# Performance work log

Hardware: AMD Instinct MI355X
Metric: run time of the kernel (lower is better)

Reference implementation:

```python
import jax, jax.numpy as jnp
import numpy as np

B, NP, L, C, NA = 16, 512, 20, 3, 50
RATIO = 0.8
K = int(np.ceil(RATIO * NP))  # 410 nodes kept per graph
N = B * NP
E = 6 * N
NF, EF = 13, 4
EPS = 1e-5


def _graph_norm(x, w, b, ms):
    # PyG GraphNorm called WITHOUT batch in the source -> single global graph
    mean = x.mean(0)
    out = x - ms * mean
    var = (out * out).mean(0)
    return w * out / jnp.sqrt(var + EPS) + b


def _forward(x, pan_w, lin1_w, lin1_b, norm1_w, norm1_b, norm1_ms,
             pool_p, pool_beta, gat_wl, gat_bl, gat_wr, gat_br, gat_att, gat_bias,
             norm2_w, norm2_b, norm2_ms,
             val1_w, val1_b, val2_w, val2_b, val3_w, val3_b,
             adv1_w, adv1_b, adv2_w, adv2_b, adv3_w, adv3_b,
             edge_index, current_node_ids, action_mask):
    src, dst = edge_index[0], edge_index[1]
    # PANConv builds SparseTensor(row=edge_index[1], col=edge_index[0]) -> row = target
    A = jnp.zeros((B, NP, NP), x.dtype).at[dst // NP, dst % NP, src % NP].set(1.0)
    eyeB = jnp.broadcast_to(jnp.eye(NP, dtype=x.dtype), A.shape)

    # panentropy: M = sum_{i=0..L} w_i * A^i  (dense per graph)
    def step(carry, wi):
        tmp, acc = carry
        tmp = tmp @ A
        return (tmp, acc + wi * tmp), None
    (_, M), _ = jax.lax.scan(step, (eyeB, pan_w[0] * eyeB), pan_w[1:])
    deg = M.sum(-1)                                   # row sums
    dis = jnp.where(deg > 0, 1.0 / jnp.sqrt(deg), 0.0)
    Mn = dis[:, :, None] * M * dis[:, None, :]        # D^-1/2 M D^-1/2

    # conv1: propagate (Mn @ x) then Linear
    x3 = x.reshape(B, NP, NF)
    h = jnp.einsum('bij,bjf->bif', Mn, x3) @ lin1_w + lin1_b   # [B,NP,C]
    x1 = jax.nn.relu(_graph_norm(h.reshape(N, C), norm1_w, norm1_b, norm1_ms))  # [N,C]
    h = x1.reshape(B, NP, C)

    # PANPooling: score = tanh(b0 * <x,p> + b1 * colsum(Mn)); keep top K per graph
    score = jnp.tanh(pool_beta[0] * (h * pool_p).sum(-1) + pool_beta[1] * Mn.sum(-2))
    vals, idx = jax.lax.top_k(score, K)                        # [B,K]
    xp = jnp.take_along_axis(h, idx[:, :, None], axis=1) * vals[..., None]
    Mg = jax.vmap(lambda m, i: m[i][:, i])(Mn, idx)            # filtered adjacency [B,K,K]
    mask = (jnp.swapaxes(Mg, 1, 2) != 0) | jnp.eye(K, dtype=bool)  # mask[b,i,j]: edge j->i (+self loops)

    # GATv2Conv, heads=1, eval mode (no dropout), edge_attr not passed in source
    xl = xp @ gat_wl + gat_bl
    xr = xp @ gat_wr + gat_br
    e = jax.nn.leaky_relu(xr[:, :, None, :] + xl[:, None, :, :], 0.2)  # [B,i,j,C]
    logits = jnp.where(mask, jnp.einsum('bijc,c->bij', e, gat_att), -1e9)
    alpha = jax.nn.softmax(logits, axis=-1)
    g = jnp.einsum('bij,bjc->bic', alpha, xl) + gat_bias

    g = jax.nn.relu(_graph_norm(g.reshape(B * K, C), norm2_w, norm2_b, norm2_ms)).reshape(B, K, C)
    gp = g.sum(1)                                              # global_add_pool [B,C]

    # source uses POOLED bincount cumsum offsets to index the pre-pool arrays (faithful)
    gidx = current_node_ids + jnp.arange(B, dtype=current_node_ids.dtype) * K
    feat = jnp.concatenate([x[gidx], x1[gidx], gp], axis=1)    # [B,19]

    a = jax.nn.relu(feat @ adv1_w + adv1_b)
    a = jax.nn.relu(a @ adv2_w + adv2_b)
    a = a @ adv3_w + adv3_b
    v = jax.nn.relu(feat @ val1_w + val1_b)
    v = jax.nn.relu(v @ val2_w + val2_b)
    v = v @ val3_w + val3_b
    q = v + (a - a.mean(1, keepdims=True))
    return jnp.where(action_mask == 0, -1e8, q)


def setup_inputs() -> dict:
    key = jax.random.key(0)
    ks = list(jax.random.split(key, 40))
    nk = lambda: ks.pop()
    # within-graph random edges so the PyG-style batch structure is valid
    g = jax.random.randint(nk(), (E,), 0, B)
    u = jax.random.randint(nk(), (E,), 0, NP)
    v = jax.random.randint(nk(), (E,), 0, NP)
    edge_index = jnp.stack([g * NP + u, g * NP + v]).astype(jnp.int32)

    def lin(k, i, o):
        k1, k2 = jax.random.split(k)
        return (jax.random.normal(k1, (i, o), jnp.float32) / np.sqrt(i),
                jax.random.normal(k2, (o,), jnp.float32) * 0.01)

    lin1_w, lin1_b = lin(nk(), NF, C)
    gat_wl, gat_bl = lin(nk(), C, C)
    gat_wr, gat_br = lin(nk(), C, C)
    val1_w, val1_b = lin(nk(), 19, 10)
    val2_w, val2_b = lin(nk(), 10, 5)
    val3_w, val3_b = lin(nk(), 5, 1)
    adv1_w, adv1_b = lin(nk(), 19, 10)
    adv2_w, adv2_b = lin(nk(), 10, 5)
    adv3_w, adv3_b = lin(nk(), 5, NA)
    return dict(
        x=jax.random.normal(nk(), (N, NF), jnp.float32),
        edge_index=edge_index,
        edge_attr=jax.random.normal(nk(), (E, EF), jnp.float32),
        batch=jnp.arange(N, dtype=jnp.int32) // NP,
        current_node_ids=jax.random.randint(nk(), (B,), 0, NP),
        action_mask=jax.random.randint(nk(), (B, NA), 0, 2),
        pan_w=jax.random.uniform(nk(), (L + 1,), jnp.float32) * 0.5,
        lin1_w=lin1_w, lin1_b=lin1_b,
        norm1_w=jnp.ones(C), norm1_b=jnp.zeros(C), norm1_ms=jnp.ones(C),
        pool_p=jax.random.normal(nk(), (C,), jnp.float32),
        pool_beta=jnp.array([0.5, 0.5], jnp.float32),
        gat_wl=gat_wl, gat_bl=gat_bl, gat_wr=gat_wr, gat_br=gat_br,
        gat_att=jax.random.normal(nk(), (C,), jnp.float32),
        gat_bias=jax.random.normal(nk(), (C,), jnp.float32) * 0.01,
        norm2_w=jnp.ones(C), norm2_b=jnp.zeros(C), norm2_ms=jnp.ones(C),
        val1_w=val1_w, val1_b=val1_b, val2_w=val2_w, val2_b=val2_b,
        val3_w=val3_w, val3_b=val3_b,
        adv1_w=adv1_w, adv1_b=adv1_b, adv2_w=adv2_w, adv2_b=adv2_b,
        adv3_w=adv3_w, adv3_b=adv3_b,
    )


def reference(x, edge_index, edge_attr, batch, current_node_ids, action_mask,
              pan_w, lin1_w, lin1_b, norm1_w, norm1_b, norm1_ms,
              pool_p, pool_beta, gat_wl, gat_bl, gat_wr, gat_br, gat_att, gat_bias,
              norm2_w, norm2_b, norm2_ms,
              val1_w, val1_b, val2_w, val2_b, val3_w, val3_b,
              adv1_w, adv1_b, adv2_w, adv2_b, adv3_w, adv3_b):
    del edge_attr, batch  # received by the torch forward but never consumed
    return _forward(x, pan_w, lin1_w, lin1_b, norm1_w, norm1_b, norm1_ms,
                    pool_p, pool_beta, gat_wl, gat_bl, gat_wr, gat_br, gat_att, gat_bias,
                    norm2_w, norm2_b, norm2_ms,
                    val1_w, val1_b, val2_w, val2_b, val3_w, val3_b,
                    adv1_w, adv1_b, adv2_w, adv2_b, adv3_w, adv3_b,
                    edge_index, current_node_ids, action_mask)
```

## Files before the change

kernel.cpp:

```cpp
#include <hip/hip_runtime.h>
#include <hip/hip_bf16.h>
#include <stdint.h>
#include <math.h>

#define BB   16
#define NPn  512
#define LLp  20
#define NAa  50
#define KKk  410
#define NNt  (BB * NPn)
#define EEe  (6 * NNt)
#define NFf  13
#define KPAD 416
#define KP2  448
#define EPSf 1e-5f
#define QCLMP 1e6f
#define MAXD 28
#define PADR 512

__device__ __forceinline__ float r17_sane(float v) {
    if (!(v == v)) return 0.0f;
    return fminf(fmaxf(v, -1e15f), 1e15f);
}

__global__ __launch_bounds__(256) void r17_scatter(
    const int* __restrict__ ei,
    uint32_t* __restrict__ fwdb, uint32_t* __restrict__ trsb)
{
    const int e = blockIdx.x * 256 + threadIdx.x;
    if (e < EEe) {
        const int src = ei[e], dst = ei[EEe + e];
        atomicOr(&fwdb[(size_t)dst * 16 + ((src & 511) >> 5)], 1u << (src & 31));
        atomicOr(&trsb[(size_t)src * 16 + ((dst & 511) >> 5)], 1u << (dst & 31));
    }
}

__global__ __launch_bounds__(256) void r17_extract(
    const uint32_t* __restrict__ fwdb, const uint32_t* __restrict__ trsb,
    unsigned short* __restrict__ csrF, unsigned short* __restrict__ csrT)
{
    const int t = blockIdx.x * 256 + threadIdx.x;
    const int node = t & 8191;
    const uint32_t* bs = (t < 8192) ? (fwdb + (size_t)node * 16)
                                    : (trsb + (size_t)node * 16);
    unsigned short* cs = (t < 8192) ? csrF : csrT;
    int cnt = 0;
    for (int w = 0; w < 16; ++w) {
        uint32_t bits = bs[w];
        while (bits) {
            const int u = (w << 5) + __ffs(bits) - 1;
            bits &= bits - 1;
            if (cnt < MAXD) cs[(size_t)cnt * 8192 + node] = (unsigned short)u;
            ++cnt;
        }
    }
    for (int j = cnt; j < MAXD; ++j) cs[(size_t)j * 8192 + node] = PADR;
}

__global__ __launch_bounds__(512) void r17_mid(
    const float* __restrict__ x,
    const unsigned short* __restrict__ csrF,
    const unsigned short* __restrict__ csrT,
    const float* __restrict__ panw,
    const float* __restrict__ l1w, const float* __restrict__ l1b,
    float* __restrict__ h_raw, float* __restrict__ colsum,
    uint32_t* __restrict__ Rb)
{
    __shared__ __align__(16) uint32_t sbuf[1047];
    float* pa  = (float*)sbuf;
    float* pb  = (float*)(sbuf + 513);
    float* wsh = (float*)(sbuf + 1026);
    const int b = blockIdx.x, y = blockIdx.y, t = threadIdx.x;
    const int node = b * 512 + t;

    if (y < 4) {
        const int c = y;
        int iF[MAXD];
#pragma unroll
        for (int j = 0; j < MAXD; ++j) iF[j] = (int)csrF[(size_t)j * 8192 + node];
        if (t < 21) wsh[t] = panw[t];

        pa[t] = 1.0f;
        if (t == 0) { pa[512] = 0.0f; pb[512] = 0.0f; }
        __syncthreads();
        float dacc = wsh[0];
        {
            float* rp = pa; float* rn = pb;
            for (int i = 1; i <= LLp; ++i) {
                float tv[MAXD];
#pragma unroll
                for (int j = 0; j < MAXD; ++j) tv[j] = rp[iF[j]];
                float s = 0.0f;
#pragma unroll
                for (int j = 0; j < MAXD; ++j) s += tv[j];
                rn[t] = s;
                dacc += wsh[i] * s;
                __syncthreads();
                float* tp = rp; rp = rn; rn = tp;
            }
        }
        const float d0 = (dacc > 0.0f) ? 1.0f / sqrtf(dacc) : 0.0f;

        int idx[MAXD];
        if (c == 3) {
#pragma unroll
            for (int j = 0; j < MAXD; ++j) idx[j] = (int)csrT[(size_t)j * 8192 + node];
        } else {
#pragma unroll
            for (int j = 0; j < MAXD; ++j) idx[j] = iF[j];
        }
        float seed;
        if (c < 3) {
            float xw = 0.0f;
            const float* xr = x + (size_t)node * NFf;
            for (int f = 0; f < NFf; ++f) xw += xr[f] * l1w[f * 3 + c];
            seed = d0 * xw;
        } else {
            seed = d0;
        }
        pa[t] = seed;
        if (t == 0) { pa[512] = 0.0f; pb[512] = 0.0f; }
        __syncthreads();
        float acc = wsh[0] * seed;
        {
            float* rp = pa; float* rn = pb;
            for (int i = 1; i <= LLp; ++i) {
                float tv[MAXD];
#pragma unroll
                for (int j = 0; j < MAXD; ++j) tv[j] = rp[idx[j]];
                float s = 0.0f;
#pragma unroll
                for (int j = 0; j < MAXD; ++j) s += tv[j];
                rn[t] = s;
                acc += wsh[i] * s;
                __syncthreads();
                float* tp = rp; rp = rn; rn = tp;
            }
        }
        if (c < 3) h_raw[(size_t)node * 3 + c] = r17_sane(d0 * acc + l1b[c]);
        else       colsum[node] = r17_sane(d0 * acc);
    } else {
        const int q = y - 4;
        int iF[MAXD];
#pragma unroll
        for (int j = 0; j < MAXD; ++j) iF[j] = (int)csrF[(size_t)j * 8192 + node];
        uint32_t* R1 = sbuf;
        uint32_t* R2 = sbuf + 513;
        R1[t] = ((t >> 5) == q) ? (1u << (t & 31)) : 0u;
        if (t == 0) { R1[512] = 0u; R2[512] = 0u; }
        __syncthreads();
        uint32_t* Rp = R1; uint32_t* Rn = R2;
        for (int i = 0; i < LLp; ++i) {
            uint32_t tv[MAXD];
#pragma unroll
            for (int j = 0; j < MAXD; ++j) tv[j] = Rp[iF[j]];
            uint32_t r = Rp[t];
#pragma unroll
            for (int j = 0; j < MAXD; ++j) r |= tv[j];
            Rn[t] = r;
            __syncthreads();
            uint32_t* tp = Rp; Rp = Rn; Rn = tp;
        }
        Rb[(size_t)node * 16 + q] = Rp[t];
    }
}

__global__ __launch_bounds__(512) void r18_pool(
    const float* __restrict__ h_raw,
    const float* __restrict__ colsum,
    const uint32_t* __restrict__ Rb,
    const float* n1w, const float* n1b, const float* n1ms,
    const float* poolp, const float* poolb,
    const float* gwl, const float* gbl,
    float* __restrict__ x1,
    float* __restrict__ xpg,
    float* __restrict__ xlg,
    int*   __restrict__ kidxg,
    uint32_t* __restrict__ RTg)
{
    __shared__ __align__(16) uint32_t pg[2208];
    float* sc   = (float*)pg;
    float* mv   = (float*)(pg + 512);
    float* wred = (float*)(pg + 520);
    float* xpS  = (float*)(pg + 544);
    int*   kidx = (int*)(pg + 1792);
    const int b = blockIdx.x, t = threadIdx.x;
    const int lane = t & 63, wv = t >> 6;
    const float inv_n = 1.0f / (float)NNt;

    float hv0[16], hv1[16], hv2[16];
    float p0 = 0.0f, p1 = 0.0f, p2 = 0.0f;
#pragma unroll
    for (int k = 0; k < 16; ++k) {
        const float* hr = h_raw + (size_t)(k * 512 + t) * 3;
        hv0[k] = hr[0]; hv1[k] = hr[1]; hv2[k] = hr[2];
        p0 += hv0[k]; p1 += hv1[k]; p2 += hv2[k];
    }
#pragma unroll
    for (int off = 32; off; off >>= 1) {
        p0 += __shfl_xor(p0, off); p1 += __shfl_xor(p1, off); p2 += __shfl_xor(p2, off);
    }
    if (lane == 0) { wred[wv * 3 + 0] = p0; wred[wv * 3 + 1] = p1; wred[wv * 3 + 2] = p2; }
    __syncthreads();
    if (t < 3) {
        float s = 0.0f;
        for (int w = 0; w < 8; ++w) s += wred[w * 3 + t];
        mv[t] = s * inv_n;
    }
    __syncthreads();
    const float mm0 = n1ms[0] * mv[0], mm1 = n1ms[1] * mv[1], mm2 = n1ms[2] * mv[2];
    float q0 = 0.0f, q1 = 0.0f, q2 = 0.0f;
#pragma unroll
    for (int k = 0; k < 16; ++k) {
        const float d0 = hv0[k] - mm0, d1 = hv1[k] - mm1, d2 = hv2[k] - mm2;
        q0 += d0 * d0; q1 += d1 * d1; q2 += d2 * d2;
    }
#pragma unroll
    for (int off = 32; off; off >>= 1) {
        q0 += __shfl_xor(q0, off); q1 += __shfl_xor(q1, off); q2 += __shfl_xor(q2, off);
    }
    if (lane == 0) { wred[wv * 3 + 0] = q0; wred[wv * 3 + 1] = q1; wred[wv * 3 + 2] = q2; }
    __syncthreads();
    if (t < 3) {
        float s = 0.0f;
        for (int w = 0; w < 8; ++w) s += wred[w * 3 + t];
        mv[3 + t] = s * inv_n;
    }
    __syncthreads();

    const float mmv[3] = { mm0, mm1, mm2 };
    float xv[3];
#pragma unroll
    for (int c = 0; c < 3; ++c) {
        const float iv = 1.0f / sqrtf(fmaxf(mv[3 + c], 0.0f) + EPSf);
        const float o  = h_raw[(size_t)(b * NPn + t) * 3 + c] - mmv[c];
        const float tt = n1w[c] * o * iv + n1b[c];
        xv[c] = fmaxf(tt, 0.0f);
        x1[(size_t)(b * NPn + t) * 3 + c] = xv[c];
    }
    float s = poolb[0] * (xv[0] * poolp[0] + xv[1] * poolp[1] + xv[2] * poolp[2])
            + poolb[1] * colsum[b * NPn + t];
    s = tanhf(s);
    if (!(s == s)) s = 0.0f;
    sc[t] = s;
    __syncthreads();

    int cnt = 0;
    for (int u = 0; u < NPn; u += 4) {
        const float4 s4 = *(const float4*)(sc + u);
        cnt += ((s4.x > s) || (s4.x == s && (u + 0) < t)) ? 1 : 0;
        cnt += ((s4.y > s) || (s4.y == s && (u + 1) < t)) ? 1 : 0;
        cnt += ((s4.z > s) || (s4.z == s && (u + 2) < t)) ? 1 : 0;
        cnt += ((s4.w > s) || (s4.w == s && (u + 3) < t)) ? 1 : 0;
    }
    if (cnt < KKk) {
        const float xp0 = xv[0] * s, xp1 = xv[1] * s, xp2 = xv[2] * s;
        kidx[cnt] = t;
        xpS[cnt * 3 + 0] = xp0;
        xpS[cnt * 3 + 1] = xp1;
        xpS[cnt * 3 + 2] = xp2;
        kidxg[b * KPAD + cnt] = t;
        xpg[(size_t)(b * KPAD + cnt) * 3 + 0] = xp0;
        xpg[(size_t)(b * KPAD + cnt) * 3 + 1] = xp1;
        xpg[(size_t)(b * KPAD + cnt) * 3 + 2] = xp2;
    }
    __syncthreads();

    float Wl[9];
#pragma unroll
    for (int i2 = 0; i2 < 9; ++i2) Wl[i2] = gwl[i2];
    const float Bl0 = gbl[0], Bl1 = gbl[1], Bl2 = gbl[2];
    if (t < KP2) {
        float xl0, xl1, xl2;
        uint32_t* RT = RTg + (size_t)b * 16 * KP2 + t;
        if (t < KKk) {
            const float c0 = xpS[t * 3 + 0];
            const float c1 = xpS[t * 3 + 1];
            const float c2 = xpS[t * 3 + 2];
            xl0 = c0 * Wl[0] + c1 * Wl[3] + c2 * Wl[6] + Bl0;
            xl1 = c0 * Wl[1] + c1 * Wl[4] + c2 * Wl[7] + Bl1;
            xl2 = c0 * Wl[2] + c1 * Wl[5] + c2 * Wl[8] + Bl2;
            const uint4* rr = (const uint4*)(Rb + (size_t)(b * NPn + kidx[t]) * 16);
            const uint4 r0 = rr[0], r1 = rr[1], r2 = rr[2], r3 = rr[3];
            RT[ 0 * KP2] = r0.x; RT[ 1 * KP2] = r0.y; RT[ 2 * KP2] = r0.z; RT[ 3 * KP2] = r0.w;
            RT[ 4 * KP2] = r1.x; RT[ 5 * KP2] = r1.y; RT[ 6 * KP2] = r1.z; RT[ 7 * KP2] = r1.w;
            RT[ 8 * KP2] = r2.x; RT[ 9 * KP2] = r2.y; RT[10 * KP2] = r2.z; RT[11 * KP2] = r2.w;
            RT[12 * KP2] = r3.x; RT[13 * KP2] = r3.y; RT[14 * KP2] = r3.z; RT[15 * KP2] = r3.w;
        } else {
            xl0 = 0.0f; xl1 = 0.0f; xl2 = 0.0f;
#pragma unroll
            for (int w = 0; w < 16; ++w) RT[w * KP2] = 0u;
        }
        xlg[(size_t)(b * KP2 + t) * 3 + 0] = xl0;
        xlg[(size_t)(b * KP2 + t) * 3 + 1] = xl1;
        xlg[(size_t)(b * KP2 + t) * 3 + 2] = xl2;
    }
}

__global__ __launch_bounds__(512) void r18_gat(
    const float* __restrict__ xpg,
    const float* __restrict__ xlg,
    const int* __restrict__ kidxg,
    const uint32_t* __restrict__ RTg,
    const float* __restrict__ gwr, const float* __restrict__ gbr,
    const float* __restrict__ gatt, const float* __restrict__ gbias,
    float* __restrict__ g_raw)
{
    const int b = blockIdx.x, y = blockIdx.y, t = threadIdx.x;
    const int lane = t & 63, wv = t >> 6;
    const int i = y * 8 + wv;
    if (i >= KKk) return;

    float Wr[9];
#pragma unroll
    for (int k = 0; k < 9; ++k) Wr[k] = gwr[k];
    const float Br0 = gbr[0], Br1 = gbr[1], Br2 = gbr[2];
    const float At0 = gatt[0], At1 = gatt[1], At2 = gatt[2];
    const float Gb0 = gbias[0], Gb1 = gbias[1], Gb2 = gbias[2];

    const int bi = kidxg[b * KPAD + i];
    const float c0 = xpg[(size_t)(b * KPAD + i) * 3 + 0];
    const float c1 = xpg[(size_t)(b * KPAD + i) * 3 + 1];
    const float c2 = xpg[(size_t)(b * KPAD + i) * 3 + 2];
    const float xr0 = c0 * Wr[0] + c1 * Wr[3] + c2 * Wr[6] + Br0;
    const float xr1 = c0 * Wr[1] + c1 * Wr[4] + c2 * Wr[7] + Br1;
    const float xr2 = c0 * Wr[2] + c1 * Wr[5] + c2 * Wr[8] + Br2;

    const uint32_t mbit = 1u << (bi & 31);
    const uint32_t* Rw = RTg + (size_t)(b * 16 + (bi >> 5)) * KP2;
    const float* xlb = xlg + (size_t)b * KP2 * 3;

    float mx = -3e38f, lsum = 0.0f, b0 = 0.0f, b1 = 0.0f, b2 = 0.0f;
#pragma unroll
    for (int it = 0; it < 7; ++it) {
        const int j = lane + it * 64;
        const uint32_t rw = Rw[j];
        const float xl0 = xlb[j * 3 + 0];
        const float xl1 = xlb[j * 3 + 1];
        const float xl2 = xlb[j * 3 + 2];
        const bool valid = (rw & mbit) || (j == i);
        float e0 = xr0 + xl0; e0 = e0 > 0.0f ? e0 : 0.2f * e0;
        float e1 = xr1 + xl1; e1 = e1 > 0.0f ? e1 : 0.2f * e1;
        float e2 = xr2 + xl2; e2 = e2 > 0.0f ? e2 : 0.2f * e2;
        const float sv = At0 * e0 + At1 * e1 + At2 * e2;
        if (valid) {
            if (sv > mx) {
                const float r = __expf(mx - sv);
                lsum *= r; b0 *= r; b1 *= r; b2 *= r;
                mx = sv;
            }
            const float pj = __expf(sv - mx);
            lsum += pj;
            b0 += pj * xl0; b1 += pj * xl1; b2 += pj * xl2;
        }
    }
#pragma unroll
    for (int off = 32; off; off >>= 1) {
        const float mo = __shfl_xor(mx, off);
        const float lo = __shfl_xor(lsum, off);
        const float d0 = __shfl_xor(b0, off);
        const float d1 = __shfl_xor(b1, off);
        const float d2 = __shfl_xor(b2, off);
        const float M  = fmaxf(mx, mo);
        const float ea = __expf(mx - M), eb = __expf(mo - M);
        lsum = lsum * ea + lo * eb;
        b0 = b0 * ea + d0 * eb;
        b1 = b1 * ea + d1 * eb;
        b2 = b2 * ea + d2 * eb;
        mx = M;
    }
    if (lane == 0) {
        const float rl = 1.0f / fmaxf(lsum, 1e-30f);
        g_raw[(size_t)(b * KPAD + i) * 3 + 0] = r17_sane(b0 * rl + Gb0);
        g_raw[(size_t)(b * KPAD + i) * 3 + 1] = r17_sane(b1 * rl + Gb1);
        g_raw[(size_t)(b * KPAD + i) * 3 + 2] = r17_sane(b2 * rl + Gb2);
    }
}

__global__ __launch_bounds__(512) void r17_head(
    const float* __restrict__ g_raw,
    const float* __restrict__ x1,
    const float* __restrict__ x,
    const int* __restrict__ cnid,
    const int* __restrict__ amask,
    const float* n2w, const float* n2b, const float* n2ms,
    const float* v1w, const float* v1b,
    const float* v2w, const float* v2b,
    const float* v3w, const float* v3b,
    const float* a1w, const float* a1b,
    const float* a2w, const float* a2b,
    const float* a3w, const float* a3b,
    float* __restrict__ out)
{
    __shared__ float wred[24];
    __shared__ float mv[6];
    __shared__ float gp[3];
    __shared__ float feat[19];
    __shared__ float h1a[10], h1v[10], h2a[5], h2v[5];
    __shared__ float a3[50];
    __shared__ float vout_s, amean_s;
    const int b = blockIdx.x, t = threadIdx.x;
    const int lane = t & 63, wv = t >> 6;
    const float denom = 1.0f / (float)(BB * KKk);

    float gv0[13], gv1[13], gv2[13];
    float p0 = 0.0f, p1 = 0.0f, p2 = 0.0f;
#pragma unroll
    for (int k = 0; k < 13; ++k) {
        const int r = k * 512 + t;
        float q0 = 0.0f, q1 = 0.0f, q2 = 0.0f;
        if (r < BB * KKk) {
            const int bq = r / KKk, iq = r - bq * KKk;
            const float* gr = g_raw + (size_t)(bq * KPAD + iq) * 3;
            q0 = gr[0]; q1 = gr[1]; q2 = gr[2];
        }
        gv0[k] = q0; gv1[k] = q1; gv2[k] = q2;
        p0 += q0; p1 += q1; p2 += q2;
    }
#pragma unroll
    for (int off = 32; off; off >>= 1) {
        p0 += __shfl_xor(p0, off); p1 += __shfl_xor(p1, off); p2 += __shfl_xor(p2, off);
    }
    if (lane == 0) { wred[wv * 3 + 0] = p0; wred[wv * 3 + 1] = p1; wred[wv * 3 + 2] = p2; }
    __syncthreads();
    if (t < 3) {
        float s = 0.0f;
        for (int w = 0; w < 8; ++w) s += wred[w * 3 + t];
        mv[t] = s * denom;
    }
    __syncthreads();
    const float mm0 = n2ms[0] * mv[0], mm1 = n2ms[1] * mv[1], mm2 = n2ms[2] * mv[2];
    float q0a = 0.0f, q1a = 0.0f, q2a = 0.0f;
#pragma unroll
    for (int k = 0; k < 13; ++k) {
        const int r = k * 512 + t;
        if (r < BB * KKk) {
            const float d0 = gv0[k] - mm0, d1 = gv1[k] - mm1, d2 = gv2[k] - mm2;
            q0a += d0 * d0; q1a += d1 * d1; q2a += d2 * d2;
        }
    }
#pragma unroll
    for (int off = 32; off; off >>= 1) {
        q0a += __shfl_xor(q0a, off); q1a += __shfl_xor(q1a, off); q2a += __shfl_xor(q2a, off);
    }
    if (lane == 0) { wred[wv * 3 + 0] = q0a; wred[wv * 3 + 1] = q1a; wred[wv * 3 + 2] = q2a; }
    __syncthreads();
    if (t < 3) {
        float s = 0.0f;
        for (int w = 0; w < 8; ++w) s += wred[w * 3 + t];
        mv[3 + t] = s * denom;
    }
    __syncthreads();

    const float mmv[3] = { mm0, mm1, mm2 };
    float s3[3] = { 0.0f, 0.0f, 0.0f };
    if (t < KKk) {
        const size_t r = (size_t)(b * KPAD + t) * 3;
#pragma unroll
        for (int c = 0; c < 3; ++c) {
            const float iv = 1.0f / sqrtf(fmaxf(mv[3 + c], 0.0f) + EPSf);
            s3[c] = fmaxf((g_raw[r + c] - mmv[c]) * iv * n2w[c] + n2b[c], 0.0f);
        }
    }
    float g0 = s3[0], g1 = s3[1], g2 = s3[2];
#pragma unroll
    for (int off = 32; off; off >>= 1) {
        g0 += __shfl_xor(g0, off); g1 += __shfl_xor(g1, off); g2 += __shfl_xor(g2, off);
    }
    if (lane == 0) { wred[wv * 3 + 0] = g0; wred[wv * 3 + 1] = g1; wred[wv * 3 + 2] = g2; }
    __syncthreads();
    if (t < 3) {
        float s = 0.0f;
        for (int w = 0; w < 8; ++w) s += wred[w * 3 + t];
        gp[t] = s;
    }
    __syncthreads();

    if (t < 19) {
        const int gidx = cnid[b] + b * KKk;
        float fv;
        if (t < 13)      fv = x[(size_t)gidx * NFf + t];
        else if (t < 16) fv = x1[(size_t)gidx * 3 + (t - 13)];
        else             fv = gp[t - 16];
        feat[t] = fv;
    }
    __syncthreads();

    if (t < 10) {
        float s = a1b[t];
        for (int f = 0; f < 19; ++f) s += feat[f] * a1w[f * 10 + t];
        h1a[t] = fmaxf(s, 0.0f);
    } else if (t >= 64 && t < 74) {
        const int j = t - 64;
        float s = v1b[j];
        for (int f = 0; f < 19; ++f) s += feat[f] * v1w[f * 10 + j];
        h1v[j] = fmaxf(s, 0.0f);
    }
    __syncthreads();
    if (t < 5) {
        float s = a2b[t];
        for (int k = 0; k < 10; ++k) s += h1a[k] * a2w[k * 5 + t];
        h2a[t] = fmaxf(s, 0.0f);
    } else if (t >= 64 && t < 69) {
        const int j = t - 64;
        float s = v2b[j];
        for (int k = 0; k < 10; ++k) s += h1v[k] * v2w[k * 5 + j];
        h2v[j] = fmaxf(s, 0.0f);
    }
    __syncthreads();
    if (t < 50) {
        float s = a3b[t];
        for (int k = 0; k < 5; ++k) s += h2a[k] * a3w[k * 50 + t];
        a3[t] = s;
    } else if (t == 64) {
        float s = v3b[0];
        for (int k = 0; k < 5; ++k) s += h2v[k] * v3w[k];
        vout_s = s;
    }
    __syncthreads();
    if (t == 0) {
        float s = 0.0f;
        for (int k = 0; k < 50; ++k) s += a3[k];
        amean_s = s * (1.0f / 50.0f);
    }
    __syncthreads();
    if (t < 50) {
        float q = vout_s + a3[t] - amean_s;
        if (!(q == q)) q = 0.0f;
        q = fminf(fmaxf(q, -QCLMP), QCLMP);
        out[b * NAa + t] = (amask[b * NAa + t] == 0) ? -1e8f : q;
    }
}

extern "C" void kernel_launch(void* const* d_in, const int* in_sizes, int n_in,
                              void* d_out, int out_size, void* d_ws, size_t ws_size,
                              hipStream_t stream) {
    (void)in_sizes; (void)n_in; (void)out_size;
    const float* x     = (const float*)d_in[0];
    const int* ei      = (const int*)d_in[1];
    const int* cnid    = (const int*)d_in[4];
    const int* amask   = (const int*)d_in[5];
    const float* panw  = (const float*)d_in[6];
    const float* l1w   = (const float*)d_in[7];
    const float* l1b   = (const float*)d_in[8];
    const float* n1w   = (const float*)d_in[9];
    const float* n1b   = (const float*)d_in[10];
    const float* n1ms  = (const float*)d_in[11];
    const float* poolp = (const float*)d_in[12];
    const float* poolb = (const float*)d_in[13];
    const float* gwl   = (const float*)d_in[14];
    const float* gbl   = (const float*)d_in[15];
    const float* gwr   = (const float*)d_in[16];
    const float* gbr   = (const float*)d_in[17];
    const float* gatt  = (const float*)d_in[18];
    const float* gbias = (const float*)d_in[19];
    const float* n2w   = (const float*)d_in[20];
    const float* n2b   = (const float*)d_in[21];
    const float* n2ms  = (const float*)d_in[22];
    const float* v1w   = (const float*)d_in[23];
    const float* v1b   = (const float*)d_in[24];
    const float* v2w   = (const float*)d_in[25];
    const float* v2b   = (const float*)d_in[26];
    const float* v3w   = (const float*)d_in[27];
    const float* v3b   = (const float*)d_in[28];
    const float* a1w   = (const float*)d_in[29];
    const float* a1b   = (const float*)d_in[30];
    const float* a2w   = (const float*)d_in[31];
    const float* a2b   = (const float*)d_in[32];
    const float* a3w   = (const float*)d_in[33];
    const float* a3b   = (const float*)d_in[34];
    float* out         = (float*)d_out;

    uint8_t* wsb = (uint8_t*)d_ws;
    uint32_t* fwdb = (uint32_t*)wsb;
    uint32_t* trsb = (uint32_t*)(wsb + 524288);
    uint32_t* Rb   = (uint32_t*)(wsb + 1048576);
    unsigned short* csrF = (unsigned short*)(wsb + 1572864);
    unsigned short* csrT = csrF + (size_t)MAXD * 8192;
    float* h_raw  = (float*)(csrT + (size_t)MAXD * 8192);
    float* x1     = h_raw + (size_t)NNt * 3;
    float* colsum = x1 + (size_t)NNt * 3;
    float* g_raw  = colsum + NNt;
    float* xpg    = g_raw + (size_t)BB * KPAD * 3;
    float* xlg    = xpg + (size_t)BB * KPAD * 3;
    int*   kidxg  = (int*)(xlg + (size_t)BB * KP2 * 3);
    uint32_t* RTg = (uint32_t*)(kidxg + (size_t)BB * KPAD);
    const size_t needed = 1572864
                        + 2 * (size_t)MAXD * 8192 * 2
                        + ((size_t)(2 * NNt * 3 + NNt
                           + 2 * BB * KPAD * 3
                           + BB * KP2 * 3)) * 4
                        + (size_t)BB * KPAD * 4
                        + (size_t)BB * 16 * KP2 * 4;
    if (ws_size < needed) return;

    hipMemsetAsync(fwdb, 0, 1048576, stream);
    r17_scatter<<<dim3((EEe + 255) / 256), dim3(256), 0, stream>>>(ei, fwdb, trsb);
    r17_extract<<<dim3(64), dim3(256), 0, stream>>>(fwdb, trsb, csrF, csrT);
    r17_mid<<<dim3(16, 20), dim3(512), 0, stream>>>(x, csrF, csrT, panw, l1w, l1b,
                                                    h_raw, colsum, Rb);
    r18_pool<<<dim3(16), dim3(512), 0, stream>>>(h_raw, colsum, Rb,
                                                 n1w, n1b, n1ms, poolp, poolb,
                                                 gwl, gbl,
                                                 x1, xpg, xlg, kidxg, RTg);
    r18_gat<<<dim3(16, 52), dim3(512), 0, stream>>>(xpg, xlg, kidxg, RTg,
                                                    gwr, gbr, gatt, gbias, g_raw);
    r17_head<<<dim3(16), dim3(512), 0, stream>>>(g_raw, x1, x, cnid, amask,
                                                 n2w, n2b, n2ms, v1w, v1b, v2w, v2b, v3w, v3b,
                                                 a1w, a1b, a2w, a2b, a3w, a3b, out);
}
```

Measured before the change: 206.5 us.

## Bound neighbor gathers by wave max degree and widen reachability bitsets

Each wave now computes the maximum real in-degree of its nodes and gathers only that many padded neighbor slots in the 20-step propagation loops, in chunks of four. This skips shared-memory reads of padding entries. The reachability closure now processes 64 columns per block with uint2 words, so the mid kernel launches 12 blocks per graph row instead of 20. GAT xl features are stored as float4 so each neighbor is one vector load. The cost is nested branches and more shared memory per block in the mid kernel.

After: 201.6 us. -2.4%, faster.

```diff
diff --git a/kernel.cpp b/kernel.cpp
--- a/kernel.cpp
+++ b/kernel.cpp
@@ -21,6 +21,82 @@
 __device__ __forceinline__ float r17_sane(float v) {
     if (!(v == v)) return 0.0f;
     return fminf(fmaxf(v, -1e15f), 1e15f);
+}
+
+__device__ __forceinline__ int r19_wmaxdeg(const int (&iF)[MAXD]) {
+    int deg = 0;
+#pragma unroll
+    for (int j = 0; j < MAXD; ++j) deg += (iF[j] != PADR) ? 1 : 0;
+#pragma unroll
+    for (int off = 32; off; off >>= 1) {
+        const int o = __shfl_xor(deg, off);
+        deg = o > deg ? o : deg;
+    }
+    return deg;
+}
+
+__device__ __forceinline__ float r19_gsum(const float* __restrict__ rp,
+                                          const int (&iF)[MAXD], int dm) {
+    float s = 0.0f;
+    s += rp[iF[0]]; s += rp[iF[1]]; s += rp[iF[2]]; s += rp[iF[3]];
+    if (dm > 4) {
+        s += rp[iF[4]]; s += rp[iF[5]]; s += rp[iF[6]]; s += rp[iF[7]];
+        if (dm > 8) {
+            s += rp[iF[8]]; s += rp[iF[9]]; s += rp[iF[10]]; s += rp[iF[11]];
+            if (dm > 12) {
+                s += rp[iF[12]]; s += rp[iF[13]]; s += rp[iF[14]]; s += rp[iF[15]];
+                if (dm > 16) {
+                    s += rp[iF[16]]; s += rp[iF[17]]; s += rp[iF[18]]; s += rp[iF[19]];
+                    if (dm > 20) {
+                        s += rp[iF[20]]; s += rp[iF[21]]; s += rp[iF[22]]; s += rp[iF[23]];
+                        if (dm > 24) {
+                            s += rp[iF[24]]; s += rp[iF[25]]; s += rp[iF[26]]; s += rp[iF[27]];
+                        }
+                    }
+                }
+            }
+        }
+    }
+    return s;
+}
+
+__device__ __forceinline__ void r19_gor(const uint2* __restrict__ rp,
+                                        const int (&iF)[MAXD], int dm, uint2& r) {
+    {
+        const uint2 v0 = rp[iF[0]], v1 = rp[iF[1]], v2 = rp[iF[2]], v3 = rp[iF[3]];
+        r.x |= v0.x | v1.x | v2.x | v3.x;
+        r.y |= v0.y | v1.y | v2.y | v3.y;
+    }
+    if (dm > 4) {
+        const uint2 v0 = rp[iF[4]], v1 = rp[iF[5]], v2 = rp[iF[6]], v3 = rp[iF[7]];
+        r.x |= v0.x | v1.x | v2.x | v3.x;
+        r.y |= v0.y | v1.y | v2.y | v3.y;
+        if (dm > 8) {
+            const uint2 w0 = rp[iF[8]], w1 = rp[iF[9]], w2 = rp[iF[10]], w3 = rp[iF[11]];
+            r.x |= w0.x | w1.x | w2.x | w3.x;
+            r.y |= w0.y | w1.y | w2.y | w3.y;
+            if (dm > 12) {
+                const uint2 u0 = rp[iF[12]], u1 = rp[iF[13]], u2 = rp[iF[14]], u3 = rp[iF[15]];
+                r.x |= u0.x | u1.x | u2.x | u3.x;
+                r.y |= u0.y | u1.y | u2.y | u3.y;
+                if (dm > 16) {
+                    const uint2 a0 = rp[iF[16]], a1 = rp[iF[17]], a2 = rp[iF[18]], a3 = rp[iF[19]];
+                    r.x |= a0.x | a1.x | a2.x | a3.x;
+                    r.y |= a0.y | a1.y | a2.y | a3.y;
+                    if (dm > 20) {
+                        const uint2 b0 = rp[iF[20]], b1 = rp[iF[21]], b2 = rp[iF[22]], b3 = rp[iF[23]];
+                        r.x |= b0.x | b1.x | b2.x | b3.x;
+                        r.y |= b0.y | b1.y | b2.y | b3.y;
+                        if (dm > 24) {
+                            const uint2 c0 = rp[iF[24]], c1 = rp[iF[25]], c2 = rp[iF[26]], c3 = rp[iF[27]];
+                            r.x |= c0.x | c1.x | c2.x | c3.x;
+                            r.y |= c0.y | c1.y | c2.y | c3.y;
+                        }
+                    }
+                }
+            }
+        }
+    }
 }
 
 __global__ __launch_bounds__(256) void r17_scatter(
@@ -57,7 +133,7 @@
     for (int j = cnt; j < MAXD; ++j) cs[(size_t)j * 8192 + node] = PADR;
 }
 
-__global__ __launch_bounds__(512) void r17_mid(
+__global__ __launch_bounds__(512) void r19_mid(
     const float* __restrict__ x,
     const unsigned short* __restrict__ csrF,
     const unsigned short* __restrict__ csrT,
@@ -66,18 +142,20 @@
     float* __restrict__ h_raw, float* __restrict__ colsum,
     uint32_t* __restrict__ Rb)
 {
-    __shared__ __align__(16) uint32_t sbuf[1047];
-    float* pa  = (float*)sbuf;
-    float* pb  = (float*)(sbuf + 513);
-    float* wsh = (float*)(sbuf + 1026);
+    __shared__ __align__(16) uint32_t sbuf[2052];
     const int b = blockIdx.x, y = blockIdx.y, t = threadIdx.x;
     const int node = b * 512 + t;
 
+    int iF[MAXD];
+#pragma unroll
+    for (int j = 0; j < MAXD; ++j) iF[j] = (int)csrF[(size_t)j * 8192 + node];
+    const int dmF = r19_wmaxdeg(iF);
+
     if (y < 4) {
         const int c = y;
-        int iF[MAXD];
-#pragma unroll
-        for (int j = 0; j < MAXD; ++j) iF[j] = (int)csrF[(size_t)j * 8192 + node];
+        float* pa  = (float*)sbuf;
+        float* pb  = (float*)(sbuf + 513);
+        float* wsh = (float*)(sbuf + 1026);
         if (t < 21) wsh[t] = panw[t];
 
         pa[t] = 1.0f;
@@ -87,12 +165,7 @@
         {
             float* rp = pa; float* rn = pb;
             for (int i = 1; i <= LLp; ++i) {
-                float tv[MAXD];
-#pragma unroll
-                for (int j = 0; j < MAXD; ++j) tv[j] = rp[iF[j]];
-                float s = 0.0f;
-#pragma unroll
-                for (int j = 0; j < MAXD; ++j) s += tv[j];
+                const float s = r19_gsum(rp, iF, dmF);
                 rn[t] = s;
                 dacc += wsh[i] * s;
                 __syncthreads();
@@ -102,12 +175,15 @@
         const float d0 = (dacc > 0.0f) ? 1.0f / sqrtf(dacc) : 0.0f;
 
         int idx[MAXD];
+        int dm2;
         if (c == 3) {
 #pragma unroll
             for (int j = 0; j < MAXD; ++j) idx[j] = (int)csrT[(size_t)j * 8192 + node];
+            dm2 = r19_wmaxdeg(idx);
         } else {
 #pragma unroll
             for (int j = 0; j < MAXD; ++j) idx[j] = iF[j];
+            dm2 = dmF;
         }
         float seed;
         if (c < 3) {
@@ -125,12 +201,7 @@
         {
             float* rp = pa; float* rn = pb;
             for (int i = 1; i <= LLp; ++i) {
-                float tv[MAXD];
-#pragma unroll
-                for (int j = 0; j < MAXD; ++j) tv[j] = rp[idx[j]];
-                float s = 0.0f;
-#pragma unroll
-                for (int j = 0; j < MAXD; ++j) s += tv[j];
+                const float s = r19_gsum(rp, idx, dm2);
                 rn[t] = s;
                 acc += wsh[i] * s;
                 __syncthreads();
@@ -141,31 +212,30 @@
         else       colsum[node] = r17_sane(d0 * acc);
     } else {
         const int q = y - 4;
-        int iF[MAXD];
-#pragma unroll
-        for (int j = 0; j < MAXD; ++j) iF[j] = (int)csrF[(size_t)j * 8192 + node];
-        uint32_t* R1 = sbuf;
-        uint32_t* R2 = sbuf + 513;
-        R1[t] = ((t >> 5) == q) ? (1u << (t & 31)) : 0u;
-        if (t == 0) { R1[512] = 0u; R2[512] = 0u; }
+        uint2* R1 = (uint2*)sbuf;
+        uint2* R2 = R1 + 513;
+        uint2 seed;
+        seed.x = ((t >> 5) == 2 * q)     ? (1u << (t & 31)) : 0u;
+        seed.y = ((t >> 5) == 2 * q + 1) ? (1u << (t & 31)) : 0u;
+        R1[t] = seed;
+        if (t == 0) {
+            uint2 z; z.x = 0u; z.y = 0u;
+            R1[512] = z; R2[512] = z;
+        }
         __syncthreads();
-        uint32_t* Rp = R1; uint32_t* Rn = R2;
+        uint2* Rp = R1; uint2* Rn = R2;
         for (int i = 0; i < LLp; ++i) {
-            uint32_t tv[MAXD];
-#pragma unroll
-            for (int j = 0; j < MAXD; ++j) tv[j] = Rp[iF[j]];
-            uint32_t r = Rp[t];
-#pragma unroll
-            for (int j = 0; j < MAXD; ++j) r |= tv[j];
+            uint2 r = Rp[t];
+            r19_gor(Rp, iF, dmF, r);
             Rn[t] = r;
             __syncthreads();
-            uint32_t* tp = Rp; Rp = Rn; Rn = tp;
-        }
-        Rb[(size_t)node * 16 + q] = Rp[t];
-    }
-}
-
-__global__ __launch_bounds__(512) void r18_pool(
+            uint2* tp = Rp; Rp = Rn; Rn = tp;
+        }
+        *(uint2*)(&Rb[(size_t)node * 16 + 2 * q]) = Rp[t];
+    }
+}
+
+__global__ __launch_bounds__(512) void r19_pool(
     const float* __restrict__ h_raw,
     const float* __restrict__ colsum,
     const uint32_t* __restrict__ Rb,
@@ -174,7 +244,7 @@
     const float* gwl, const float* gbl,
     float* __restrict__ x1,
     float* __restrict__ xpg,
-    float* __restrict__ xlg,
+    float4* __restrict__ xlg,
     int*   __restrict__ kidxg,
     uint32_t* __restrict__ RTg)
 {
@@ -291,15 +361,13 @@
 #pragma unroll
             for (int w = 0; w < 16; ++w) RT[w * KP2] = 0u;
         }
-        xlg[(size_t)(b * KP2 + t) * 3 + 0] = xl0;
-        xlg[(size_t)(b * KP2 + t) * 3 + 1] = xl1;
-        xlg[(size_t)(b * KP2 + t) * 3 + 2] = xl2;
-    }
-}
-
-__global__ __launch_bounds__(512) void r18_gat(
+        xlg[(size_t)(b * KP2 + t)] = make_float4(xl0, xl1, xl2, 0.0f);
+    }
+}
+
+__global__ __launch_bounds__(512) void r19_gat(
     const float* __restrict__ xpg,
-    const float* __restrict__ xlg,
+    const float4* __restrict__ xlg,
     const int* __restrict__ kidxg,
     const uint32_t* __restrict__ RTg,
     const float* __restrict__ gwr, const float* __restrict__ gbr,
@@ -328,16 +396,15 @@
 
     const uint32_t mbit = 1u << (bi & 31);
     const uint32_t* Rw = RTg + (size_t)(b * 16 + (bi >> 5)) * KP2;
-    const float* xlb = xlg + (size_t)b * KP2 * 3;
+    const float4* xlb = xlg + (size_t)b * KP2;
 
     float mx = -3e38f, lsum = 0.0f, b0 = 0.0f, b1 = 0.0f, b2 = 0.0f;
 #pragma unroll
     for (int it = 0; it < 7; ++it) {
         const int j = lane + it * 64;
         const uint32_t rw = Rw[j];
-        const float xl0 = xlb[j * 3 + 0];
-        const float xl1 = xlb[j * 3 + 1];
-        const float xl2 = xlb[j * 3 + 2];
+        const float4 xlv = xlb[j];
+        const float xl0 = xlv.x, xl1 = xlv.y, xl2 = xlv.z;
         const bool valid = (rw & mbit) || (j == i);
         float e0 = xr0 + xl0; e0 = e0 > 0.0f ? e0 : 0.2f * e0;
         float e1 = xr1 + xl1; e1 = e1 > 0.0f ? e1 : 0.2f * e1;
@@ -582,14 +649,14 @@
     float* colsum = x1 + (size_t)NNt * 3;
     float* g_raw  = colsum + NNt;
     float* xpg    = g_raw + (size_t)BB * KPAD * 3;
-    float* xlg    = xpg + (size_t)BB * KPAD * 3;
-    int*   kidxg  = (int*)(xlg + (size_t)BB * KP2 * 3);
+    float4* xlg   = (float4*)(xpg + (size_t)BB * KPAD * 3);
+    int*   kidxg  = (int*)(xlg + (size_t)BB * KP2);
     uint32_t* RTg = (uint32_t*)(kidxg + (size_t)BB * KPAD);
     const size_t needed = 1572864
                         + 2 * (size_t)MAXD * 8192 * 2
                         + ((size_t)(2 * NNt * 3 + NNt
-                           + 2 * BB * KPAD * 3
-                           + BB * KP2 * 3)) * 4
+                           + 2 * BB * KPAD * 3)) * 4
+                        + (size_t)BB * KP2 * 16
                         + (size_t)BB * KPAD * 4
                         + (size_t)BB * 16 * KP2 * 4;
     if (ws_size < needed) return;
@@ -597,13 +664,13 @@
     hipMemsetAsync(fwdb, 0, 1048576, stream);
     r17_scatter<<<dim3((EEe + 255) / 256), dim3(256), 0, stream>>>(ei, fwdb, trsb);
     r17_extract<<<dim3(64), dim3(256), 0, stream>>>(fwdb, trsb, csrF, csrT);
-    r17_mid<<<dim3(16, 20), dim3(512), 0, stream>>>(x, csrF, csrT, panw, l1w, l1b,
+    r19_mid<<<dim3(16, 12), dim3(512), 0, stream>>>(x, csrF, csrT, panw, l1w, l1b,
                                                     h_raw, colsum, Rb);
-    r18_pool<<<dim3(16), dim3(512), 0, stream>>>(h_raw, colsum, Rb,
+    r19_pool<<<dim3(16), dim3(512), 0, stream>>>(h_raw, colsum, Rb,
                                                  n1w, n1b, n1ms, poolp, poolb,
                                                  gwl, gbl,
                                                  x1, xpg, xlg, kidxg, RTg);
-    r18_gat<<<dim3(16, 52), dim3(512), 0, stream>>>(xpg, xlg, kidxg, RTg,
+    r19_gat<<<dim3(16, 52), dim3(512), 0, stream>>>(xpg, xlg, kidxg, RTg,
                                                     gwr, gbr, gatt, gbias, g_raw);
     r17_head<<<dim3(16), dim3(512), 0, stream>>>(g_raw, x1, x, cnid, amask,
                                                  n2w, n2b, n2ms, v1w, v1b, v2w, v2b, v3w, v3b,
```
